# Kernel tuning notes

Hardware: AMD Instinct MI355X
Metric: run time of the kernel (lower is better)

The kernel has to match this reference:

```python
import jax, jax.numpy as jnp
import numpy as np

EPS = 1e-5   # BatchNorm eps
TAU = 0.1    # gumbel-softmax temperature (self.temperature)
N_LOCAL = 32 # max_local_num
B, M, D, S = 4, 8192, 64, 1024
MLP = [32, 128]


def setup_inputs() -> dict:
    key = jax.random.key(0)
    ks = jax.random.split(key, 12)
    coordinate = jax.random.normal(ks[0], (B, M, 3), dtype=jnp.float32)
    feature = jax.random.normal(ks[1], (B, M, D), dtype=jnp.float32)
    u = jax.random.uniform(ks[2], (B, S, M), dtype=jnp.float32, minval=1e-6, maxval=1.0 - 1e-6)
    gumbel_noise = -jnp.log(-jnp.log(u))
    w0 = jax.random.normal(ks[3], (5, MLP[0]), dtype=jnp.float32) * (1.0 / np.sqrt(5))
    w1 = jax.random.normal(ks[4], (MLP[0], MLP[1]), dtype=jnp.float32) * (1.0 / np.sqrt(MLP[0]))
    w2 = jax.random.normal(ks[5], (MLP[1], S), dtype=jnp.float32) * (1.0 / np.sqrt(MLP[1]))
    bn0_gamma = 1.0 + 0.1 * jax.random.normal(ks[6], (MLP[0],), dtype=jnp.float32)
    bn0_beta = 0.1 * jax.random.normal(ks[7], (MLP[0],), dtype=jnp.float32)
    bn0_mean = 0.1 * jax.random.normal(ks[8], (MLP[0],), dtype=jnp.float32)
    bn0_var = jax.random.uniform(ks[9], (MLP[0],), dtype=jnp.float32, minval=0.5, maxval=1.5)
    bn1_gamma = 1.0 + 0.1 * jax.random.normal(ks[10], (MLP[1],), dtype=jnp.float32)
    bn1_beta = 0.1 * jax.random.normal(ks[11], (MLP[1],), dtype=jnp.float32)
    k2 = jax.random.split(jax.random.fold_in(key, 7), 2)
    bn1_mean = 0.1 * jax.random.normal(k2[0], (MLP[1],), dtype=jnp.float32)
    bn1_var = jax.random.uniform(k2[1], (MLP[1],), dtype=jnp.float32, minval=0.5, maxval=1.5)
    return dict(coordinate=coordinate, feature=feature, gumbel_noise=gumbel_noise,
                w0=w0, bn0_gamma=bn0_gamma, bn0_beta=bn0_beta, bn0_mean=bn0_mean, bn0_var=bn0_var,
                w1=w1, bn1_gamma=bn1_gamma, bn1_beta=bn1_beta, bn1_mean=bn1_mean, bn1_var=bn1_var,
                w2=w2)


def _bn(x, gamma, beta, mean, var):
    # BatchNorm1d in inference form over the channel (last) dim
    return (x - mean) * jax.lax.rsqrt(var + EPS) * gamma + beta


def reference(coordinate, feature, gumbel_noise,
              w0, bn0_gamma, bn0_beta, bn0_mean, bn0_var,
              w1, bn1_gamma, bn1_beta, bn1_mean, bn1_var,
              w2):
    # spherical features: [x, y, z, theta, phi] -> [B, m, 5]
    r = jnp.linalg.norm(coordinate, axis=-1)
    th = jnp.arccos(coordinate[..., 2] / r)
    fi = jnp.arctan2(coordinate[..., 1], coordinate[..., 0])
    c2 = jnp.concatenate([coordinate, th[..., None], fi[..., None]], axis=-1)
    # per-point MLP with BN + ReLU
    h = jax.nn.relu(_bn(c2 @ w0, bn0_gamma, bn0_beta, bn0_mean, bn0_var))
    h = jax.nn.relu(_bn(h @ w1, bn1_gamma, bn1_beta, bn1_mean, bn1_var))
    logits = h @ w2                        # [B, m, s]
    Q = jax.nn.sigmoid(jnp.swapaxes(logits, 1, 2))  # [B, s, m]
    # topk grouping over points
    _, idx = jax.lax.top_k(Q, N_LOCAL)     # [B, s, n]
    b_idx = jnp.arange(coordinate.shape[0])[:, None, None]
    grouped_points = coordinate[b_idx, idx]   # [B, s, n, 3]
    grouped_feature = feature[b_idx, idx]     # [B, s, n, d]
    # gumbel-softmax (hard, straight-through) sampling over points
    y_soft = jax.nn.softmax((Q + gumbel_noise) / TAU, axis=-1)
    hard_idx = jnp.argmax(y_soft, axis=-1)
    y_hard = jax.nn.one_hot(hard_idx, Q.shape[-1], dtype=Q.dtype)
    Qg = y_hard - jax.lax.stop_gradient(y_soft) + y_soft  # [B, s, m]
    sampled_points = Qg @ coordinate        # [B, s, 3]
    sampled_feature = Qg @ feature          # [B, s, d]
    grouped_feature = grouped_feature.at[:, :, 0, :].set(sampled_feature)
    return sampled_points, grouped_points, sampled_feature, grouped_feature, Qg
```

## Files before the change

kernel.cpp:

```cpp
#include <hip/hip_runtime.h>
#include <math.h>

#define Bd   4
#define Md   8192
#define Dd   64
#define Sd   1024
#define H0d  32
#define H1d  128

#define OFF_SP 0
#define OFF_GP 12288
#define OFF_SF 405504
#define OFF_GF 667648
#define OFF_QG 9056256

#define CAP 512

__device__ __forceinline__ unsigned f2u(float f) {
    unsigned v = __float_as_uint(f);
    return (v & 0x80000000u) ? ~v : (v | 0x80000000u);
}

__global__ __launch_bounds__(256) void k1_mlp(
    const float* __restrict__ coord,
    const float* __restrict__ w0,
    const float* __restrict__ g0, const float* __restrict__ be0,
    const float* __restrict__ mu0, const float* __restrict__ va0,
    const float* __restrict__ w1,
    const float* __restrict__ g1, const float* __restrict__ be1,
    const float* __restrict__ mu1, const float* __restrict__ va1,
    float* __restrict__ h1T)
{
    __shared__ double W1[H0d * H1d];
    __shared__ double W0[5 * H0d];
    __shared__ double MU0[H0d], RS0[H0d], BE0[H0d];
    __shared__ double MU1[H1d], RS1[H1d], BE1[H1d];
    const int t = threadIdx.x;
    for (int i = t; i < H0d * H1d; i += 256) W1[i] = (double)w1[i];
    if (t < 5 * H0d) W0[t] = (double)w0[t];
    if (t < H0d) {
        MU0[t] = (double)mu0[t];
        RS0[t] = (double)g0[t] / sqrt((double)va0[t] + 1e-5);
        BE0[t] = (double)be0[t];
    }
    if (t >= 128) {
        int j = t - 128;
        MU1[j] = (double)mu1[j];
        RS1[j] = (double)g1[j] / sqrt((double)va1[j] + 1e-5);
        BE1[j] = (double)be1[j];
    }
    __syncthreads();

    const int p = blockIdx.x * 256 + t;
    const double x = (double)coord[p * 3 + 0];
    const double y = (double)coord[p * 3 + 1];
    const double z = (double)coord[p * 3 + 2];
    const double r  = sqrt(x * x + y * y + z * z);
    const double th = acos(z / r);
    const double fi = atan2(y, x);

    double h0[H0d];
    #pragma unroll
    for (int i = 0; i < H0d; i++) {
        double a = x * W0[i] + y * W0[H0d + i] + z * W0[2 * H0d + i]
                 + th * W0[3 * H0d + i] + fi * W0[4 * H0d + i];
        a = (a - MU0[i]) * RS0[i] + BE0[i];
        h0[i] = a > 0.0 ? a : 0.0;
    }
    float* o = h1T + (size_t)(p >> 13) * (H1d * Md) + (p & (Md - 1));
    for (int j = 0; j < H1d; j += 2) {
        double a0 = 0.0, a1 = 0.0;
        #pragma unroll
        for (int i = 0; i < H0d; i++) {
            double h = h0[i];
            a0 += h * W1[i * H1d + j];
            a1 += h * W1[i * H1d + j + 1];
        }
        a0 = (a0 - MU1[j]) * RS1[j] + BE1[j];             a0 = a0 > 0.0 ? a0 : 0.0;
        a1 = (a1 - MU1[j + 1]) * RS1[j + 1] + BE1[j + 1]; a1 = a1 > 0.0 ? a1 : 0.0;
        o[(size_t)j * Md]       = (float)a0;
        o[(size_t)(j + 1) * Md] = (float)a1;
    }
}

__global__ __launch_bounds__(256, 4) void k2_gemm(
    const float* __restrict__ h1T,
    const float* __restrict__ w2,
    float* __restrict__ logits)
{
    __shared__ float As[32][128];
    __shared__ float Bs[32][128];
    const int bx = blockIdx.x, b = blockIdx.y;
    const int mtile = bx & 63, stile = bx >> 6;
    const int m0 = mtile * 128, s0 = stile * 128;
    const int t = threadIdx.x;
    const int tm = t & 15, tn = t >> 4;

    float acc[8][8] = {};

    for (int kt = 0; kt < 4; kt++) {
        const float* Ag = h1T + ((size_t)b * H1d + kt * 32) * Md + m0;
        const float* Bg = w2 + (size_t)(kt * 32) * Sd + s0;
        #pragma unroll
        for (int i = 0; i < 4; i++) {
            int idx = t + i * 256;
            int kk = idx >> 5, c = idx & 31;
            *(float4*)&As[kk][c * 4] = *(const float4*)&Ag[(size_t)kk * Md + c * 4];
            *(float4*)&Bs[kk][c * 4] = *(const float4*)&Bg[(size_t)kk * Sd + c * 4];
        }
        __syncthreads();

        #pragma unroll 8
        for (int k = 0; k < 32; k++) {
            float a_[8], b_[8];
            *(float4*)&a_[0] = *(const float4*)&As[k][tm * 4];
            *(float4*)&a_[4] = *(const float4*)&As[k][64 + tm * 4];
            *(float4*)&b_[0] = *(const float4*)&Bs[k][tn * 4];
            *(float4*)&b_[4] = *(const float4*)&Bs[k][64 + tn * 4];
            #pragma unroll
            for (int si = 0; si < 8; si++)
                #pragma unroll
                for (int mi = 0; mi < 8; mi++)
                    acc[si][mi] += b_[si] * a_[mi];
        }
        __syncthreads();
    }

    #pragma unroll
    for (int si = 0; si < 8; si++) {
        int s = s0 + (si >> 2) * 64 + tn * 4 + (si & 3);
        float* row = logits + ((size_t)b * Sd + s) * Md + m0;
        *(float4*)&row[tm * 4]      = make_float4(acc[si][0], acc[si][1], acc[si][2], acc[si][3]);
        *(float4*)&row[64 + tm * 4] = make_float4(acc[si][4], acc[si][5], acc[si][6], acc[si][7]);
    }
}

__global__ __launch_bounds__(256) void k3_fused(
    float* __restrict__ logits,
    const float* __restrict__ gumbel,
    const float* __restrict__ coord,
    const float* __restrict__ feat,
    float* __restrict__ out)
{
    const int r = blockIdx.x;
    const int b = r >> 10;
    const int t = threadIdx.x;
    const int lane = t & 63, wav = t >> 6;
    const float4* L4 = (const float4*)(logits + (size_t)r * Md);
    const float4* G4 = (const float4*)(gumbel + (size_t)r * Md);

    __shared__ unsigned long long wred[2][4];
    __shared__ unsigned long long ck[CAP];
    __shared__ unsigned swT[4];
    __shared__ int cnt;
    __shared__ int order[32];

    unsigned uq[32];
    unsigned gbu = 0u; int gbm = 0;
    #pragma unroll
    for (int j = 0; j < 8; j++) {
        float4 v = L4[j * 256 + t];
        float4 g = G4[j * 256 + t];
        #pragma unroll
        for (int c = 0; c < 4; c++) {
            float x = ((const float*)&v)[c];
            float q = 1.0f / (1.0f + expf(-x));
            uq[j * 4 + c] = f2u(q);
            unsigned us = f2u(q + ((const float*)&g)[c]);
            if (us > gbu) { gbu = us; gbm = j * 1024 + t * 4 + c; }
        }
    }

    {
        unsigned long long key = ((unsigned long long)gbu << 32) | (unsigned)(Md - 1 - gbm);
        #pragma unroll
        for (int o = 32; o > 0; o >>= 1) {
            unsigned long long other = __shfl_down(key, o);
            if (other > key) key = other;
        }
        if (lane == 0) wred[0][wav] = key;
    }
    if (t == 0) cnt = 0;
    __syncthreads();
    unsigned long long gbest = wred[0][0];
    if (wred[0][1] > gbest) gbest = wred[0][1];
    if (wred[0][2] > gbest) gbest = wred[0][2];
    if (wred[0][3] > gbest) gbest = wred[0][3];
    const int am = Md - 1 - (int)(gbest & 0xFFFFFFFFull);

    unsigned pm = 0u;
    #pragma unroll
    for (int i = 0; i < 32; i++) pm = max(pm, uq[i]);
    unsigned v = pm;
    #pragma unroll
    for (int k = 2; k <= 64; k <<= 1) {
        #pragma unroll
        for (int j = k >> 1; j > 0; j >>= 1) {
            unsigned o = __shfl_xor(v, j);
            bool up = ((lane & k) == 0);
            bool lower = ((lane & j) == 0);
            unsigned mn = min(v, o), mx = max(v, o);
            v = (lower == up) ? mn : mx;
        }
    }
    unsigned tw = __shfl(v, 32);
    if (lane == 0) swT[wav] = tw;
    __syncthreads();
    const unsigned T = max(max(swT[0], swT[1]), max(swT[2], swT[3]));

    #pragma unroll
    for (int i = 0; i < 32; i++) {
        if (uq[i] >= T) {
            int pos = atomicAdd(&cnt, 1);
            if (pos < CAP) {
                int m = (i >> 2) * 1024 + t * 4 + (i & 3);
                ck[pos] = ((unsigned long long)uq[i] << 32) | (unsigned)(Md - 1 - m);
            }
        }
    }
    __syncthreads();
    const int n = cnt;

    if (n >= 32 && n <= CAP) {
        for (int j2 = t; j2 < n; j2 += 256) {
            unsigned long long mine = ck[j2];
            int rk = 0;
            for (int i2 = 0; i2 < n; i2++) rk += (ck[i2] > mine) ? 1 : 0;
            if (rk < 32) order[rk] = Md - 1 - (int)(mine & 0xFFFFFFFFull);
        }
    } else {
        for (int round = 0; round < 32; round++) {
            unsigned bu = 0u; int bi = 0;
            #pragma unroll
            for (int i = 0; i < 32; i++)
                if (uq[i] > bu) { bu = uq[i]; bi = i; }
            int bm = (bi >> 2) * 1024 + t * 4 + (bi & 3);
            unsigned long long key =
                ((unsigned long long)bu << 32) | (unsigned)(Md - 1 - bm);
            #pragma unroll
            for (int o = 32; o > 0; o >>= 1) {
                unsigned long long other = __shfl_down(key, o);
                if (other > key) key = other;
            }
            const int p = round & 1;
            if (lane == 0) wred[p][wav] = key;
            __syncthreads();
            unsigned long long best = wred[p][0];
            if (wred[p][1] > best) best = wred[p][1];
            if (wred[p][2] > best) best = wred[p][2];
            if (wred[p][3] > best) best = wred[p][3];
            const int m_win = Md - 1 - (int)(best & 0xFFFFFFFFull);
            if (((m_win >> 2) & 255) == t)
                uq[(m_win >> 10) * 4 + (m_win & 3)] = 0u;
            if (t == 0) order[round] = m_win;
        }
    }
    __syncthreads();

    {
        const int q4 = am >> 2;
        float4* row = (float4*)(logits + (size_t)r * Md);
        #pragma unroll
        for (int i = 0; i < 8; i++) {
            int idx = i * 256 + t;
            float4 vv = make_float4(0.f, 0.f, 0.f, 0.f);
            if (idx == q4) ((float*)&vv)[am & 3] = 1.0f;
            row[idx] = vv;
        }
    }
    if (t < 3)
        out[OFF_SP + (size_t)r * 3 + t] = coord[((size_t)b * Md + am) * 3 + t];
    if (t >= 32 && t < 128) {
        int e = t - 32;
        int nn = e / 3, c = e - nn * 3;
        out[OFF_GP + (size_t)r * 96 + e] = coord[((size_t)b * Md + order[nn]) * 3 + c];
    }
    const float4* F4  = (const float4*)feat;
    float4* SF4 = (float4*)(out + OFF_SF);
    float4* GF4 = (float4*)(out + OFF_GF);
    if (t < 16) {
        float4 fv = F4[((size_t)b * Md + am) * 16 + t];
        SF4[(size_t)r * 16 + t]  = fv;
        GF4[(size_t)r * 512 + t] = fv;
    }
    for (int e4 = 16 + t; e4 < 512; e4 += 256) {
        int nn = e4 >> 4, d4 = e4 & 15;
        GF4[(size_t)r * 512 + e4] = F4[((size_t)b * Md + order[nn]) * 16 + d4];
    }
}

extern "C" void kernel_launch(void* const* d_in, const int* in_sizes, int n_in,
                              void* d_out, int out_size, void* d_ws, size_t ws_size,
                              hipStream_t stream)
{
    (void)in_sizes; (void)n_in; (void)out_size; (void)d_ws; (void)ws_size;
    const float* coord = (const float*)d_in[0];
    const float* feat  = (const float*)d_in[1];
    const float* gum   = (const float*)d_in[2];
    const float* w0    = (const float*)d_in[3];
    const float* g0    = (const float*)d_in[4];
    const float* be0   = (const float*)d_in[5];
    const float* mu0   = (const float*)d_in[6];
    const float* va0   = (const float*)d_in[7];
    const float* w1    = (const float*)d_in[8];
    const float* g1    = (const float*)d_in[9];
    const float* be1   = (const float*)d_in[10];
    const float* mu1   = (const float*)d_in[11];
    const float* va1   = (const float*)d_in[12];
    const float* w2    = (const float*)d_in[13];

    float*  out    = (float*)d_out;
    float*  h1T    = out + OFF_GF;
    float*  logits = out + OFF_QG;

    k1_mlp   <<<dim3(128),     dim3(256), 0, stream>>>(coord, w0, g0, be0, mu0, va0,
                                                       w1, g1, be1, mu1, va1, h1T);
    k2_gemm  <<<dim3(512, 4),  dim3(256), 0, stream>>>(h1T, w2, logits);
    k3_fused <<<dim3(4096),    dim3(256), 0, stream>>>(logits, gum, coord, feat, out);
}
```

Before: 226.6 us.

## Split MLP output channels across blocks and move sigmoid into GEMM epilogue

The per-point MLP kernel now launches four blocks per point tile, each computing 32 of the 128 hidden channels with a quarter-size double-precision weight table, so the 128-block launch becomes 512 blocks and fills more of the device. The layer-0 work and the coordinate trig are repeated in each of the four blocks. Separately, the GEMM epilogue applies the sigmoid and stores order-preserving unsigned keys, and the fused top-k kernel reads those keys directly instead of recomputing the sigmoid. That moves the exp work into the GEMM epilogue, with an unchanged total amount of exp.

```diff
diff --git a/kernel.cpp b/kernel.cpp
--- a/kernel.cpp
+++ b/kernel.cpp
@@ -31,27 +31,32 @@
     const float* __restrict__ mu1, const float* __restrict__ va1,
     float* __restrict__ h1T)
 {
-    __shared__ double W1[H0d * H1d];
+    const int jg = blockIdx.x & 3;
+    const int j0 = jg * 32;
+    __shared__ double W1[H0d * 32];
     __shared__ double W0[5 * H0d];
     __shared__ double MU0[H0d], RS0[H0d], BE0[H0d];
-    __shared__ double MU1[H1d], RS1[H1d], BE1[H1d];
+    __shared__ double MU1[32], RS1[32], BE1[32];
     const int t = threadIdx.x;
-    for (int i = t; i < H0d * H1d; i += 256) W1[i] = (double)w1[i];
+    for (int e = t; e < H0d * 32; e += 256) {
+        int i = e >> 5, jc = e & 31;
+        W1[e] = (double)w1[i * H1d + j0 + jc];
+    }
     if (t < 5 * H0d) W0[t] = (double)w0[t];
     if (t < H0d) {
         MU0[t] = (double)mu0[t];
         RS0[t] = (double)g0[t] / sqrt((double)va0[t] + 1e-5);
         BE0[t] = (double)be0[t];
     }
-    if (t >= 128) {
-        int j = t - 128;
-        MU1[j] = (double)mu1[j];
-        RS1[j] = (double)g1[j] / sqrt((double)va1[j] + 1e-5);
-        BE1[j] = (double)be1[j];
-    }
-    __syncthreads();
-
-    const int p = blockIdx.x * 256 + t;
+    if (t >= 192 && t < 224) {
+        int j = t - 192;
+        MU1[j] = (double)mu1[j0 + j];
+        RS1[j] = (double)g1[j0 + j] / sqrt((double)va1[j0 + j] + 1e-5);
+        BE1[j] = (double)be1[j0 + j];
+    }
+    __syncthreads();
+
+    const int p = (blockIdx.x >> 2) * 256 + t;
     const double x = (double)coord[p * 3 + 0];
     const double y = (double)coord[p * 3 + 1];
     const double z = (double)coord[p * 3 + 2];
@@ -68,25 +73,25 @@
         h0[i] = a > 0.0 ? a : 0.0;
     }
     float* o = h1T + (size_t)(p >> 13) * (H1d * Md) + (p & (Md - 1));
-    for (int j = 0; j < H1d; j += 2) {
+    for (int jc = 0; jc < 32; jc += 2) {
         double a0 = 0.0, a1 = 0.0;
         #pragma unroll
         for (int i = 0; i < H0d; i++) {
             double h = h0[i];
-            a0 += h * W1[i * H1d + j];
-            a1 += h * W1[i * H1d + j + 1];
-        }
-        a0 = (a0 - MU1[j]) * RS1[j] + BE1[j];             a0 = a0 > 0.0 ? a0 : 0.0;
-        a1 = (a1 - MU1[j + 1]) * RS1[j + 1] + BE1[j + 1]; a1 = a1 > 0.0 ? a1 : 0.0;
-        o[(size_t)j * Md]       = (float)a0;
-        o[(size_t)(j + 1) * Md] = (float)a1;
+            a0 += h * W1[i * 32 + jc];
+            a1 += h * W1[i * 32 + jc + 1];
+        }
+        a0 = (a0 - MU1[jc]) * RS1[jc] + BE1[jc];             a0 = a0 > 0.0 ? a0 : 0.0;
+        a1 = (a1 - MU1[jc + 1]) * RS1[jc + 1] + BE1[jc + 1]; a1 = a1 > 0.0 ? a1 : 0.0;
+        o[(size_t)(j0 + jc) * Md]     = (float)a0;
+        o[(size_t)(j0 + jc + 1) * Md] = (float)a1;
     }
 }
 
 __global__ __launch_bounds__(256, 4) void k2_gemm(
     const float* __restrict__ h1T,
     const float* __restrict__ w2,
-    float* __restrict__ logits)
+    unsigned* __restrict__ uqout)
 {
     __shared__ float As[32][128];
     __shared__ float Bs[32][128];
@@ -129,14 +134,23 @@
     #pragma unroll
     for (int si = 0; si < 8; si++) {
         int s = s0 + (si >> 2) * 64 + tn * 4 + (si & 3);
-        float* row = logits + ((size_t)b * Sd + s) * Md + m0;
-        *(float4*)&row[tm * 4]      = make_float4(acc[si][0], acc[si][1], acc[si][2], acc[si][3]);
-        *(float4*)&row[64 + tm * 4] = make_float4(acc[si][4], acc[si][5], acc[si][6], acc[si][7]);
+        unsigned* row = uqout + ((size_t)b * Sd + s) * Md + m0;
+        uint4 w0v, w1v;
+        w0v.x = f2u(1.0f / (1.0f + expf(-acc[si][0])));
+        w0v.y = f2u(1.0f / (1.0f + expf(-acc[si][1])));
+        w0v.z = f2u(1.0f / (1.0f + expf(-acc[si][2])));
+        w0v.w = f2u(1.0f / (1.0f + expf(-acc[si][3])));
+        w1v.x = f2u(1.0f / (1.0f + expf(-acc[si][4])));
+        w1v.y = f2u(1.0f / (1.0f + expf(-acc[si][5])));
+        w1v.z = f2u(1.0f / (1.0f + expf(-acc[si][6])));
+        w1v.w = f2u(1.0f / (1.0f + expf(-acc[si][7])));
+        *(uint4*)&row[tm * 4]      = w0v;
+        *(uint4*)&row[64 + tm * 4] = w1v;
     }
 }
 
 __global__ __launch_bounds__(256) void k3_fused(
-    float* __restrict__ logits,
+    unsigned* __restrict__ uqbuf,
     const float* __restrict__ gumbel,
     const float* __restrict__ coord,
     const float* __restrict__ feat,
@@ -146,7 +160,7 @@
     const int b = r >> 10;
     const int t = threadIdx.x;
     const int lane = t & 63, wav = t >> 6;
-    const float4* L4 = (const float4*)(logits + (size_t)r * Md);
+    const uint4*  L4 = (const uint4*)(uqbuf + (size_t)r * Md);
     const float4* G4 = (const float4*)(gumbel + (size_t)r * Md);
 
     __shared__ unsigned long long wred[2][4];
@@ -159,13 +173,13 @@
     unsigned gbu = 0u; int gbm = 0;
     #pragma unroll
     for (int j = 0; j < 8; j++) {
-        float4 v = L4[j * 256 + t];
+        uint4  v = L4[j * 256 + t];
         float4 g = G4[j * 256 + t];
         #pragma unroll
         for (int c = 0; c < 4; c++) {
-            float x = ((const float*)&v)[c];
-            float q = 1.0f / (1.0f + expf(-x));
-            uq[j * 4 + c] = f2u(q);
+            unsigned u = ((const unsigned*)&v)[c];
+            uq[j * 4 + c] = u;
+            float q = __uint_as_float(u ^ 0x80000000u);
             unsigned us = f2u(q + ((const float*)&g)[c]);
             if (us > gbu) { gbu = us; gbm = j * 1024 + t * 4 + c; }
         }
@@ -259,7 +273,7 @@
 
     {
         const int q4 = am >> 2;
-        float4* row = (float4*)(logits + (size_t)r * Md);
+        float4* row = (float4*)(uqbuf + (size_t)r * Md);
         #pragma unroll
         for (int i = 0; i < 8; i++) {
             int idx = i * 256 + t;
@@ -309,12 +323,12 @@
     const float* va1   = (const float*)d_in[12];
     const float* w2    = (const float*)d_in[13];
 
-    float*  out    = (float*)d_out;
-    float*  h1T    = out + OFF_GF;
-    float*  logits = out + OFF_QG;
-
-    k1_mlp   <<<dim3(128),     dim3(256), 0, stream>>>(coord, w0, g0, be0, mu0, va0,
+    float*    out  = (float*)d_out;
+    float*    h1T  = out + OFF_GF;
+    unsigned* uqb  = (unsigned*)(out + OFF_QG);
+
+    k1_mlp   <<<dim3(512),     dim3(256), 0, stream>>>(coord, w0, g0, be0, mu0, va0,
                                                        w1, g1, be1, mu1, va1, h1T);
-    k2_gemm  <<<dim3(512, 4),  dim3(256), 0, stream>>>(h1T, w2, logits);
-    k3_fused <<<dim3(4096),    dim3(256), 0, stream>>>(logits, gum, coord, feat, out);
-}
+    k2_gemm  <<<dim3(512, 4),  dim3(256), 0, stream>>>(h1T, w2, uqb);
+    k3_fused <<<dim3(4096),    dim3(256), 0, stream>>>(uqb, gum, coord, feat, out);
+}
```

Result: no change. 229.9 us (+1.5%).
